# Kernel optimization log

Hardware: AMD Instinct MI355X
Metric: run time of the kernel (lower is better)

## Reference

```python
import jax, jax.numpy as jnp
import numpy as np

B, S, D_IN, D_QK, D_V = 4, 4096, 1024, 64, 64

def setup_inputs() -> dict:
    key = jax.random.key(0)
    ks = jax.random.split(key, 8)
    sd = 1.0 / np.sqrt(D_IN)
    return {
        "X": jax.random.normal(ks[0], (B, S, D_IN), dtype=jnp.float32),
        "mask": jnp.ones((B, S, 1), dtype=jnp.float32),
        "Wq": jax.random.uniform(ks[1], (D_IN, D_QK), jnp.float32, -sd, sd),
        "bq": jax.random.uniform(ks[2], (D_QK,), jnp.float32, -sd, sd),
        "Wk": jax.random.uniform(ks[3], (D_IN, D_QK), jnp.float32, -sd, sd),
        "bk": jax.random.uniform(ks[4], (D_QK,), jnp.float32, -sd, sd),
        "Wv": jax.random.uniform(ks[5], (D_IN, D_V), jnp.float32, -sd, sd),
        "bv": jax.random.uniform(ks[6], (D_V,), jnp.float32, -sd, sd),
    }

def reference(X, mask, Wq, bq, Wk, bk, Wv, bv):
    # ReLU-activated projections (no head split, no 1/sqrt(d) scaling)
    q = jax.nn.relu(jnp.einsum('bsd,df->bsf', X, Wq) + bq)   # [B,S,D_QK]
    k = jax.nn.relu(jnp.einsum('bsd,df->bsf', X, Wk) + bk)   # [B,S,D_QK]
    v = jax.nn.relu(jnp.einsum('bsd,df->bsf', X, Wv) + bv)   # [B,S,D_V]
    scores = jax.nn.softmax(jnp.einsum('bqf,bkf->bqk', q, k), axis=-1)  # [B,S,S]
    return jnp.einsum('bqk,bkf->bqf', scores, v) * mask       # mask applied AFTER AV
```

## Files before the change

kernel.cpp:

```cpp
#include <hip/hip_runtime.h>


typedef short s16x8 __attribute__((ext_vector_type(8)));
typedef _Float16 f16x8 __attribute__((ext_vector_type(8)));
typedef float fx4   __attribute__((ext_vector_type(4)));
typedef unsigned short u16x4 __attribute__((ext_vector_type(4)));

#define LOG2E 1.4426950408889634f

__device__ __forceinline__ unsigned short f2bf(float x) {
    unsigned int u = __float_as_uint(x);
    u += 0x7FFFu + ((u >> 16) & 1u);
    return (unsigned short)(u >> 16);
}
__device__ __forceinline__ float bf2f(unsigned short b) {
    return __uint_as_float(((unsigned int)b) << 16);
}

__global__ __launch_bounds__(256) void prep_kernel(
    const float* __restrict__ X,
    const float* __restrict__ Wq, const float* __restrict__ Wk, const float* __restrict__ Wv,
    _Float16* __restrict__ wt_h, _Float16* __restrict__ xt)
{
    __shared__ __align__(16) _Float16 sh[64][72];
    const int bid = blockIdx.x;
    const int t   = threadIdx.x;

    if (bid < 48) {
        const int y  = bid >> 4;
        const int kt = bid & 15;
        const float* W = (y == 0) ? Wq : (y == 1) ? Wk : Wv;

        const int kl = t >> 2;
        const int c0 = (t & 3) * 16;
        const float* src = W + (size_t)(kt * 64 + kl) * 64 + c0;
        #pragma unroll
        for (int j = 0; j < 4; j++) {
            fx4 v = *(const fx4*)(src + j * 4);
            #pragma unroll
            for (int i = 0; i < 4; i++)
                sh[c0 + j * 4 + i][kl] = (_Float16)v[i];
        }
        __syncthreads();

        const int c  = t >> 2;
        const int k0 = (t & 3) * 16;
        size_t o = (size_t)(y * 64 + c) * 1024 + kt * 64 + k0;
        *(f16x8*)(wt_h + o)     = *(const f16x8*)&sh[c][k0];
        *(f16x8*)(wt_h + o + 8) = *(const f16x8*)&sh[c][k0 + 8];
    } else {
        const int xb   = bid - 48;
        const int tile = xb >> 2;
        const int qrt  = xb & 3;
        const int rl   = t >> 6;
        const int c    = (t & 63) * 16;
        const int kc   = c >> 6;
        const int kk   = c & 63;

        #pragma unroll
        for (int it = 0; it < 4; it++) {
            int row = qrt * 16 + it * 4 + rl;
            const float* src = X + (((size_t)(tile * 64 + row)) << 10) + c;
            _Float16 h[16];
            #pragma unroll
            for (int j = 0; j < 4; j++) {
                fx4 v = *(const fx4*)(src + j * 4);
                #pragma unroll
                for (int i = 0; i < 4; i++)
                    h[j * 4 + i] = (_Float16)v[i];
            }
            _Float16* dst = xt + ((((size_t)tile * 16 + kc) * 64 + row) << 6) + kk;
            *(f16x8*)dst       = *(const f16x8*)&h[0];
            *(f16x8*)(dst + 8) = *(const f16x8*)&h[8];
        }
    }
}

__global__ __launch_bounds__(256, 4) void proj_kernel(
    const _Float16* __restrict__ xt, const _Float16* __restrict__ wt_h,
    const float* __restrict__ bq, const float* __restrict__ bk, const float* __restrict__ bv,
    unsigned short* __restrict__ q_hi, unsigned short* __restrict__ q_lo,
    unsigned short* __restrict__ k_bf, unsigned short* __restrict__ vt_g)
{
    __shared__ __align__(16) _Float16 wls[64][264];

    const int tid  = threadIdx.x;
    const int lane = tid & 63;
    const int w    = tid >> 6;
    const int quad = lane >> 4;
    const int l15  = lane & 15;

    const int f   = blockIdx.x;
    const int xcd = f & 7;
    const int jj  = f >> 3;
    const int y   = jj % 3;
    const int mt  = (jj / 3) * 8 + xcd;
    const int m0  = mt * 64;

    const _Float16* xtb = xt + (((size_t)mt * 16) * 64 + (w * 16 + l15)) * 64 + quad * 8;

    const int wcol = tid >> 2;
    const int wk0  = (tid & 3) * 64;
    const size_t wgb = (size_t)(y * 64 + wcol) * 1024 + wk0;

    f16x8 wr[8];
    #pragma unroll
    for (int i = 0; i < 8; i++)
        wr[i] = *(const f16x8*)(wt_h + wgb + i * 8);

    f16x8 xc0 = *(const f16x8*)(xtb);
    f16x8 xc1 = *(const f16x8*)(xtb + 32);

    fx4 acc[4];
    #pragma unroll
    for (int nt = 0; nt < 4; nt++) acc[nt] = (fx4){0.f, 0.f, 0.f, 0.f};

    for (int ch = 0; ch < 4; ch++) {
        if (ch) __syncthreads();
        #pragma unroll
        for (int i = 0; i < 8; i++)
            *(f16x8*)&wls[wcol][wk0 + i * 8] = wr[i];
        __syncthreads();
        if (ch < 3) {
            #pragma unroll
            for (int i = 0; i < 8; i++)
                wr[i] = *(const f16x8*)(wt_h + wgb + (ch + 1) * 256 + i * 8);
        }

        #pragma unroll
        for (int kk = 0; kk < 4; kk++) {
            const int kc = ch * 4 + kk;
            f16x8 xn0, xn1;
            if (kc < 15) {
                xn0 = *(const f16x8*)(xtb + (kc + 1) * 4096);
                xn1 = *(const f16x8*)(xtb + (kc + 1) * 4096 + 32);
            }
            #pragma unroll
            for (int nt = 0; nt < 4; nt++) {
                const int ko = kk * 64 + quad * 8;
                f16x8 b0 = *(const f16x8*)&wls[nt * 16 + l15][ko];
                f16x8 b1 = *(const f16x8*)&wls[nt * 16 + l15][ko + 32];
                acc[nt] = __builtin_amdgcn_mfma_f32_16x16x32_f16(xc0, b0, acc[nt], 0, 0, 0);
                acc[nt] = __builtin_amdgcn_mfma_f32_16x16x32_f16(xc1, b1, acc[nt], 0, 0, 0);
            }
            xc0 = xn0; xc1 = xn1;
        }
    }
    __syncthreads();

    const float* bias = (y == 0) ? bq : (y == 1) ? bk : bv;

    unsigned short* vtr = (unsigned short*)&wls[0][0];

    #pragma unroll
    for (int nt = 0; nt < 4; nt++) {
        int col = nt * 16 + l15;
        float bb = bias[col];
        int rloc = w * 16 + quad * 4;
        #pragma unroll
        for (int r = 0; r < 4; r++) {
            float v = acc[nt][r] + bb;
            v = fmaxf(v, 0.f);
            size_t grow = (size_t)(m0 + rloc + r);
            if (y == 0) {
                unsigned short h = f2bf(v);
                unsigned short l = f2bf(v - bf2f(h));
                q_hi[grow * 64 + col] = h;
                q_lo[grow * 64 + col] = l;
            } else if (y == 1) {
                k_bf[grow * 64 + col] = f2bf(v);
            } else {
                vtr[col * 72 + rloc + r] = f2bf(v);
            }
        }
    }
    if (y == 2) {
        __syncthreads();
        int rowd = tid >> 2;
        int off  = (tid & 3) * 16;
        s16x8 v0 = *(const s16x8*)&vtr[rowd * 72 + off];
        s16x8 v1 = *(const s16x8*)&vtr[rowd * 72 + off + 8];
        unsigned short* dst = vt_g + ((size_t)mt * 64 + rowd) * 64 + off;
        *(s16x8*)(dst)     = v0;
        *(s16x8*)(dst + 8) = v1;
    }
}

__global__ __launch_bounds__(256, 6) void attn_kernel(
    const unsigned short* __restrict__ q_hi, const unsigned short* __restrict__ q_lo,
    const unsigned short* __restrict__ k_bf, const unsigned short* __restrict__ vt_g,
    unsigned short* __restrict__ pOb, float* __restrict__ pL)
{
    __shared__ __align__(16) unsigned short kt[64][72];
    __shared__ __align__(16) unsigned short vt[64][72];
    __shared__ __align__(16) unsigned short pt[4][16][40];

    const int tid  = threadIdx.x;
    const int lane = tid & 63;
    const int w    = tid >> 6;
    const int quad = lane >> 4;
    const int l15  = lane & 15;
    const int ck   = blockIdx.y;
    const int b    = blockIdx.z;
    const int q0   = blockIdx.x * 64;

    const size_t qoff = ((size_t)b * 4096 + q0 + w * 16 + l15) * 64 + quad * 8;
    s16x8 qh0 = *(const s16x8*)(q_hi + qoff);
    s16x8 qh1 = *(const s16x8*)(q_hi + qoff + 32);
    s16x8 ql0 = *(const s16x8*)(q_lo + qoff);
    s16x8 ql1 = *(const s16x8*)(q_lo + qoff + 32);

    fx4 accO[4];
    #pragma unroll
    for (int nt = 0; nt < 4; nt++) accO[nt] = (fx4){0.f, 0.f, 0.f, 0.f};
    float lsum[4] = {0.f, 0.f, 0.f, 0.f};

    const unsigned short* kgb = k_bf + (size_t)b * 4096 * 64;
    const unsigned short* vgb = vt_g + (size_t)b * 64 * 4096;

    const int srow = tid >> 3;
    const int soff = (tid & 7) * 8;

    s16x8 kr[2], vr[2];
    {
        const int it0 = ck * 8;
        const unsigned short* kg = kgb + (size_t)it0 * 4096;
        const unsigned short* vg = vgb + (size_t)it0 * 4096;
        #pragma unroll
        for (int i = 0; i < 2; i++) {
            int row = srow + i * 32;
            kr[i] = *(const s16x8*)(kg + (size_t)row * 64 + soff);
            vr[i] = *(const s16x8*)(vg + (size_t)row * 64 + soff);
        }
    }

    for (int i2 = 0; i2 < 8; i2++) {
        const int it = ck * 8 + i2;
        if (i2) __syncthreads();
        #pragma unroll
        for (int i = 0; i < 2; i++) {
            int row = srow + i * 32;
            *(s16x8*)&kt[row][soff] = kr[i];
            *(s16x8*)&vt[row][soff] = vr[i];
        }
        __syncthreads();
        if (i2 < 7) {
            const unsigned short* kg = kgb + (size_t)(it + 1) * 4096;
            const unsigned short* vg = vgb + (size_t)(it + 1) * 4096;
            #pragma unroll
            for (int i = 0; i < 2; i++) {
                int row = srow + i * 32;
                kr[i] = *(const s16x8*)(kg + (size_t)row * 64 + soff);
                vr[i] = *(const s16x8*)(vg + (size_t)row * 64 + soff);
            }
        }

        #pragma unroll
        for (int kh = 0; kh < 2; kh++) {
            #pragma unroll
            for (int nt2 = 0; nt2 < 2; nt2++) {
                int key = kh * 32 + nt2 * 16 + l15;
                s16x8 k0 = *(const s16x8*)&kt[key][quad * 8];
                s16x8 k1 = *(const s16x8*)&kt[key][32 + quad * 8];
                fx4 sc = (fx4){0.f, 0.f, 0.f, 0.f};
                sc = __builtin_amdgcn_mfma_f32_16x16x32_bf16(qh0, k0, sc, 0, 0, 0);
                sc = __builtin_amdgcn_mfma_f32_16x16x32_bf16(ql0, k0, sc, 0, 0, 0);
                sc = __builtin_amdgcn_mfma_f32_16x16x32_bf16(qh1, k1, sc, 0, 0, 0);
                sc = __builtin_amdgcn_mfma_f32_16x16x32_bf16(ql1, k1, sc, 0, 0, 0);
                #pragma unroll
                for (int r = 0; r < 4; r++) {
                    float p = __builtin_amdgcn_exp2f(sc[r] * LOG2E);
                    unsigned short pb = f2bf(p);
                    lsum[r] += bf2f(pb);
                    pt[w][quad * 4 + r][nt2 * 16 + l15] = pb;
                }
            }
            s16x8 pa = *(const s16x8*)&pt[w][l15][quad * 8];
            #pragma unroll
            for (int nt = 0; nt < 4; nt++) {
                s16x8 vf = *(const s16x8*)&vt[nt * 16 + l15][kh * 32 + quad * 8];
                accO[nt] = __builtin_amdgcn_mfma_f32_16x16x32_bf16(pa, vf, accO[nt], 0, 0, 0);
            }
        }
    }

    #pragma unroll
    for (int r = 0; r < 4; r++) {
        float v = lsum[r];
        #pragma unroll
        for (int o = 1; o < 16; o <<= 1) v += __shfl_xor(v, o);
        lsum[r] = v;
    }
    #pragma unroll
    for (int r = 0; r < 4; r++) {
        int qrow = q0 + w * 16 + quad * 4 + r;
        size_t grow = (size_t)b * 4096 + qrow;
        #pragma unroll
        for (int nt = 0; nt < 4; nt++)
            pOb[((size_t)ck * 16384 + grow) * 64 + nt * 16 + l15] = f2bf(accO[nt][r]);
        if (l15 == 0)
            pL[(size_t)ck * 16384 + grow] = lsum[r];
    }
}

__global__ __launch_bounds__(256) void combine_kernel(
    const unsigned short* __restrict__ pOb, const float* __restrict__ pL,
    const float* __restrict__ mask, float* __restrict__ out)
{
    int idx = blockIdx.x * 256 + threadIdx.x;
    int q  = idx >> 4;
    int dg = idx & 15;
    fx4 s = (fx4){0.f, 0.f, 0.f, 0.f};
    float l = 0.f;
    #pragma unroll
    for (int c = 0; c < 8; c++) {
        u16x4 h = *(const u16x4*)(pOb + ((size_t)c * 16384 + q) * 64 + dg * 4);
        s.x += bf2f(h.x);
        s.y += bf2f(h.y);
        s.z += bf2f(h.z);
        s.w += bf2f(h.w);
        l += pL[(size_t)c * 16384 + q];
    }
    float scale = mask[q] / l;
    *(fx4*)(out + (size_t)q * 64 + dg * 4) = s * scale;
}

extern "C" void kernel_launch(void* const* d_in, const int* in_sizes, int n_in,
                              void* d_out, int out_size, void* d_ws, size_t ws_size,
                              hipStream_t stream)
{
    const float* X    = (const float*)d_in[0];
    const float* mask = (const float*)d_in[1];
    const float* Wq   = (const float*)d_in[2];
    const float* bq   = (const float*)d_in[3];
    const float* Wk   = (const float*)d_in[4];
    const float* bk   = (const float*)d_in[5];
    const float* Wv   = (const float*)d_in[6];
    const float* bv   = (const float*)d_in[7];
    float* out = (float*)d_out;

    char* ws = (char*)d_ws;
    unsigned short* q_hi  = (unsigned short*)(ws);
    unsigned short* q_lo  = (unsigned short*)(ws + (size_t)(2u << 20));
    unsigned short* k_bf  = (unsigned short*)(ws + (size_t)(4u << 20));
    unsigned short* vt_g  = (unsigned short*)(ws + (size_t)(6u << 20));
    _Float16*       wt_h  = (_Float16*)(ws + (size_t)(8u << 20));
    _Float16*       xt    = (_Float16*)(ws + (size_t)(9u << 20));
    unsigned short* pOb   = (unsigned short*)(ws + (size_t)(9u << 20));
    float*          pL    = (float*)(ws + (size_t)(41u << 20));

    hipLaunchKernelGGL(prep_kernel, dim3(1072), dim3(256), 0, stream,
                       X, Wq, Wk, Wv, wt_h, xt);
    hipLaunchKernelGGL(proj_kernel, dim3(768), dim3(256), 0, stream,
                       xt, wt_h, bq, bk, bv, q_hi, q_lo, k_bf, vt_g);
    hipLaunchKernelGGL(attn_kernel, dim3(64, 8, 4), dim3(256), 0, stream,
                       q_hi, q_lo, k_bf, vt_g, pOb, pL);
    hipLaunchKernelGGL(combine_kernel, dim3(1024), dim3(256), 0, stream,
                       pOb, pL, mask, out);
}
```

Baseline: 179.4 us.

## Load K/V fragments directly from global into registers and compute row sums via MFMA

The attention kernel stops staging K and V tiles through LDS with block-wide barriers. Each wave now loads its MFMA fragments for K and V straight from global memory into registers every iteration. The softmax denominator is computed with an extra MFMA against a ones vector instead of per-lane accumulation and shuffle reductions. Occupancy hint drops from 6 to 4 blocks to make room for the larger register footprint. The trade is redundant global/L2 traffic across the four waves and no prefetch overlap, in exchange for fewer barriers and less LDS traffic.

```diff
diff --git a/kernel.cpp b/kernel.cpp
--- a/kernel.cpp
+++ b/kernel.cpp
@@ -149,7 +149,6 @@
     __syncthreads();
 
     const float* bias = (y == 0) ? bq : (y == 1) ? bk : bv;
-
     unsigned short* vtr = (unsigned short*)&wls[0][0];
 
     #pragma unroll
@@ -186,14 +185,12 @@
     }
 }
 
-__global__ __launch_bounds__(256, 6) void attn_kernel(
+__global__ __launch_bounds__(256, 4) void attn_kernel(
     const unsigned short* __restrict__ q_hi, const unsigned short* __restrict__ q_lo,
     const unsigned short* __restrict__ k_bf, const unsigned short* __restrict__ vt_g,
     unsigned short* __restrict__ pOb, float* __restrict__ pL)
 {
-    __shared__ __align__(16) unsigned short kt[64][72];
-    __shared__ __align__(16) unsigned short vt[64][72];
-    __shared__ __align__(16) unsigned short pt[4][16][40];
+    __shared__ unsigned short pt[4][16][36];
 
     const int tid  = threadIdx.x;
     const int lane = tid & 63;
@@ -210,87 +207,58 @@
     s16x8 ql0 = *(const s16x8*)(q_lo + qoff);
     s16x8 ql1 = *(const s16x8*)(q_lo + qoff + 32);
 
+    s16x8 ones;
+    #pragma unroll
+    for (int i = 0; i < 8; i++) ones[i] = (short)0x3F80;
+
     fx4 accO[4];
     #pragma unroll
     for (int nt = 0; nt < 4; nt++) accO[nt] = (fx4){0.f, 0.f, 0.f, 0.f};
-    float lsum[4] = {0.f, 0.f, 0.f, 0.f};
+    fx4 accL = (fx4){0.f, 0.f, 0.f, 0.f};
 
     const unsigned short* kgb = k_bf + (size_t)b * 4096 * 64;
     const unsigned short* vgb = vt_g + (size_t)b * 64 * 4096;
 
-    const int srow = tid >> 3;
-    const int soff = (tid & 7) * 8;
-
-    s16x8 kr[2], vr[2];
-    {
-        const int it0 = ck * 8;
-        const unsigned short* kg = kgb + (size_t)it0 * 4096;
-        const unsigned short* vg = vgb + (size_t)it0 * 4096;
-        #pragma unroll
-        for (int i = 0; i < 2; i++) {
-            int row = srow + i * 32;
-            kr[i] = *(const s16x8*)(kg + (size_t)row * 64 + soff);
-            vr[i] = *(const s16x8*)(vg + (size_t)row * 64 + soff);
-        }
-    }
-
     for (int i2 = 0; i2 < 8; i2++) {
         const int it = ck * 8 + i2;
-        if (i2) __syncthreads();
-        #pragma unroll
-        for (int i = 0; i < 2; i++) {
-            int row = srow + i * 32;
-            *(s16x8*)&kt[row][soff] = kr[i];
-            *(s16x8*)&vt[row][soff] = vr[i];
-        }
-        __syncthreads();
-        if (i2 < 7) {
-            const unsigned short* kg = kgb + (size_t)(it + 1) * 4096;
-            const unsigned short* vg = vgb + (size_t)(it + 1) * 4096;
-            #pragma unroll
-            for (int i = 0; i < 2; i++) {
-                int row = srow + i * 32;
-                kr[i] = *(const s16x8*)(kg + (size_t)row * 64 + soff);
-                vr[i] = *(const s16x8*)(vg + (size_t)row * 64 + soff);
-            }
+        const unsigned short* kg = kgb + (size_t)it * 4096;
+        const unsigned short* vg = vgb + (size_t)it * 4096;
+
+        s16x8 kf[4][2], vf[4][2];
+        #pragma unroll
+        for (int g = 0; g < 4; g++) {
+            const unsigned short* kr = kg + (size_t)(g * 16 + l15) * 64 + quad * 8;
+            const unsigned short* vr = vg + (size_t)(g * 16 + l15) * 64 + quad * 8;
+            kf[g][0] = *(const s16x8*)(kr);
+            kf[g][1] = *(const s16x8*)(kr + 32);
+            vf[g][0] = *(const s16x8*)(vr);
+            vf[g][1] = *(const s16x8*)(vr + 32);
         }
 
         #pragma unroll
         for (int kh = 0; kh < 2; kh++) {
             #pragma unroll
             for (int nt2 = 0; nt2 < 2; nt2++) {
-                int key = kh * 32 + nt2 * 16 + l15;
-                s16x8 k0 = *(const s16x8*)&kt[key][quad * 8];
-                s16x8 k1 = *(const s16x8*)&kt[key][32 + quad * 8];
+                const int g = kh * 2 + nt2;
                 fx4 sc = (fx4){0.f, 0.f, 0.f, 0.f};
-                sc = __builtin_amdgcn_mfma_f32_16x16x32_bf16(qh0, k0, sc, 0, 0, 0);
-                sc = __builtin_amdgcn_mfma_f32_16x16x32_bf16(ql0, k0, sc, 0, 0, 0);
-                sc = __builtin_amdgcn_mfma_f32_16x16x32_bf16(qh1, k1, sc, 0, 0, 0);
-                sc = __builtin_amdgcn_mfma_f32_16x16x32_bf16(ql1, k1, sc, 0, 0, 0);
+                sc = __builtin_amdgcn_mfma_f32_16x16x32_bf16(qh0, kf[g][0], sc, 0, 0, 0);
+                sc = __builtin_amdgcn_mfma_f32_16x16x32_bf16(ql0, kf[g][0], sc, 0, 0, 0);
+                sc = __builtin_amdgcn_mfma_f32_16x16x32_bf16(qh1, kf[g][1], sc, 0, 0, 0);
+                sc = __builtin_amdgcn_mfma_f32_16x16x32_bf16(ql1, kf[g][1], sc, 0, 0, 0);
                 #pragma unroll
                 for (int r = 0; r < 4; r++) {
                     float p = __builtin_amdgcn_exp2f(sc[r] * LOG2E);
-                    unsigned short pb = f2bf(p);
-                    lsum[r] += bf2f(pb);
-                    pt[w][quad * 4 + r][nt2 * 16 + l15] = pb;
+                    pt[w][quad * 4 + r][nt2 * 16 + l15] = f2bf(p);
                 }
             }
             s16x8 pa = *(const s16x8*)&pt[w][l15][quad * 8];
             #pragma unroll
-            for (int nt = 0; nt < 4; nt++) {
-                s16x8 vf = *(const s16x8*)&vt[nt * 16 + l15][kh * 32 + quad * 8];
-                accO[nt] = __builtin_amdgcn_mfma_f32_16x16x32_bf16(pa, vf, accO[nt], 0, 0, 0);
-            }
-        }
-    }
-
-    #pragma unroll
-    for (int r = 0; r < 4; r++) {
-        float v = lsum[r];
-        #pragma unroll
-        for (int o = 1; o < 16; o <<= 1) v += __shfl_xor(v, o);
-        lsum[r] = v;
-    }
+            for (int nt = 0; nt < 4; nt++)
+                accO[nt] = __builtin_amdgcn_mfma_f32_16x16x32_bf16(pa, vf[nt][kh], accO[nt], 0, 0, 0);
+            accL = __builtin_amdgcn_mfma_f32_16x16x32_bf16(pa, ones, accL, 0, 0, 0);
+        }
+    }
+
     #pragma unroll
     for (int r = 0; r < 4; r++) {
         int qrow = q0 + w * 16 + quad * 4 + r;
@@ -299,7 +267,7 @@
         for (int nt = 0; nt < 4; nt++)
             pOb[((size_t)ck * 16384 + grow) * 64 + nt * 16 + l15] = f2bf(accO[nt][r]);
         if (l15 == 0)
-            pL[(size_t)ck * 16384 + grow] = lsum[r];
+            pL[(size_t)ck * 16384 + grow] = accL[r];
     }
 }
 
```

Measured after the change: 277.5 us. 54.7% more time.
